# Kernel tuning notes

Measured on AMD Instinct MI355X. Metric: run time of the kernel, lower is better.

Reference implementation:

```python
import jax, jax.numpy as jnp
import numpy as np

B, S, HID = 2, 2048, 768
NH, HD = 12, 64
WINDOW_HALF = 64  # local_attention // 2
ROPE_THETA = 10000.0  # local_rope_theta (layer_id=1 -> local layer)


def setup_inputs() -> dict:
    key = jax.random.key(0)
    k1, k2, k3 = jax.random.split(key, 3)
    hidden_states = jax.random.normal(k1, (B, S, HID), dtype=jnp.float32)
    Wqkv_w = jax.random.normal(k2, (3 * HID, HID), dtype=jnp.float32) * (1.0 / np.sqrt(HID))
    Wo_w = jax.random.normal(k3, (HID, HID), dtype=jnp.float32) * (1.0 / np.sqrt(HID))
    # additive sliding-window mask: 0 inside +/-WINDOW_HALF band, finfo.min outside
    idx = jnp.arange(S)
    band = jnp.abs(idx[:, None] - idx[None, :]) <= WINDOW_HALF
    neg = jnp.finfo(jnp.float32).min
    sliding_window_mask = jnp.where(band, 0.0, neg)[None, None, :, :].astype(jnp.float32)
    position_ids = jnp.tile(jnp.arange(S, dtype=jnp.int64)[None, :], (B, 1))
    return {
        "hidden_states": hidden_states,
        "Wqkv_w": Wqkv_w,
        "Wo_w": Wo_w,
        "sliding_window_mask": sliding_window_mask,
        "position_ids": position_ids,
    }


def _rotate_half(x):
    x1, x2 = jnp.split(x, 2, axis=-1)
    return jnp.concatenate((-x2, x1), axis=-1)


def _rope_cos_sin(position_ids):
    # inv_freq: [HD//2]
    inv_freq = 1.0 / (ROPE_THETA ** (jnp.arange(0, HD, 2, dtype=jnp.float32) / HD))
    freqs = position_ids.astype(jnp.float32)[:, :, None] * inv_freq[None, None, :]  # [B,S,HD//2]
    emb = jnp.concatenate((freqs, freqs), axis=-1)  # [B,S,HD]
    return jnp.cos(emb), jnp.sin(emb)


def reference(hidden_states, Wqkv_w, Wo_w, sliding_window_mask, position_ids):
    bs, s, _ = hidden_states.shape
    qkv = hidden_states @ Wqkv_w.T  # [B,S,3*HID]
    qkv = qkv.reshape(bs, s, 3, NH, HD)
    # transpose(3,1).unbind(2) -> q,k,v each [B,NH,S,HD]
    qkv = jnp.transpose(qkv, (0, 3, 2, 1, 4))
    q, k, v = qkv[:, :, 0], qkv[:, :, 1], qkv[:, :, 2]
    cos, sin = _rope_cos_sin(position_ids)  # [B,S,HD]
    cos = cos[:, None, :, :].astype(hidden_states.dtype)
    sin = sin[:, None, :, :].astype(hidden_states.dtype)
    q = q * cos + _rotate_half(q) * sin
    k = k * cos + _rotate_half(k) * sin
    scale = 1.0 / np.sqrt(HD)
    scores = jnp.einsum("bhqd,bhkd->bhqk", q, k) * scale + sliding_window_mask
    probs = jax.nn.softmax(scores, axis=-1)
    attn = jnp.einsum("bhqk,bhkd->bhqd", probs, v)  # [B,NH,S,HD]
    attn = jnp.transpose(attn, (0, 2, 1, 3)).reshape(bs, s, NH * HD)
    return attn @ Wo_w.T
```

## Files before the change

### kernel.cpp

```cpp
#include <hip/hip_runtime.h>
#include <hip/hip_bf16.h>
#include <cstdint>

typedef __bf16 bf16_t;
typedef __bf16 bf16x8 __attribute__((ext_vector_type(8)));
typedef float f32x4 __attribute__((ext_vector_type(4)));

#define B_    2
#define S_    2048
#define HID_  768
#define NH_   12
#define HD_   64
#define KDIM_ 768

#define N_HID_  3145728
#define N_WQKV_ 1769472
#define N_WO_   589824

__device__ __forceinline__ void glds16(const bf16_t* g, const bf16_t* lds) {
  __builtin_amdgcn_global_load_lds((const __attribute__((address_space(1))) void*)g,
                                   (__attribute__((address_space(3))) void*)lds,
                                   16, 0, 0);
}

__global__ __launch_bounds__(256) void cvt3_kernel(
    const float* __restrict__ a, const float* __restrict__ b, const float* __restrict__ c,
    bf16_t* __restrict__ da, bf16_t* __restrict__ db, bf16_t* __restrict__ dc)
{
  size_t i = ((size_t)blockIdx.x * 256 + threadIdx.x) * 8;
  const float* s; bf16_t* d; size_t off;
  if (i < N_HID_)                { s = a; d = da; off = i; }
  else if (i < N_HID_ + N_WQKV_) { s = b; d = db; off = i - N_HID_; }
  else                           { s = c; d = dc; off = i - (N_HID_ + N_WQKV_); }
  float4 v0 = *(const float4*)(s + off);
  float4 v1 = *(const float4*)(s + off + 4);
  bf16x8 o;
  o[0] = (bf16_t)v0.x; o[1] = (bf16_t)v0.y; o[2] = (bf16_t)v0.z; o[3] = (bf16_t)v0.w;
  o[4] = (bf16_t)v1.x; o[5] = (bf16_t)v1.y; o[6] = (bf16_t)v1.z; o[7] = (bf16_t)v1.w;
  *(bf16x8*)(d + off) = o;
}

template<int MODE, int BM, int BN, int WM, int WN, int NTHR, int MINW, int NTX, int CHUNK>
__launch_bounds__(NTHR, MINW)
__global__ void gemm_kernel(const bf16_t* __restrict__ A,
                            const bf16_t* __restrict__ Bw,
                            bf16_t* __restrict__ Qo,
                            bf16_t* __restrict__ Ko,
                            bf16_t* __restrict__ Vo,
                            float* __restrict__ outf)
{
  constexpr int W    = WM * WN;
  constexpr int MACC = BM / WM / 16;
  constexpr int NWF  = BN / WN / 16;
  __shared__ bf16_t As[BM * 64];
  __shared__ bf16_t Bs[BN * 64];

  const int tid  = threadIdx.x;
  const int w    = tid >> 6;
  const int lane = tid & 63;
  const int wm   = w / WN, wn = w % WN;
  const int wk = (blockIdx.x & 7) * CHUNK + (blockIdx.x >> 3);
  const int tx = wk % NTX, ty = wk / NTX;
  const int m0 = ty * BM;
  const int n0 = tx * BN;
  const int lr  = lane >> 3;
  const int sub = lane & 7;

  f32x4 acc[MACC][NWF];
#pragma unroll
  for (int i = 0; i < MACC; i++)
#pragma unroll
    for (int j = 0; j < NWF; j++) acc[i][j] = f32x4{0.f, 0.f, 0.f, 0.f};

  for (int k0 = 0; k0 < KDIM_; k0 += 64) {
#pragma unroll
    for (int q = 0; q < BM / 8 / W; ++q) {
      const int rb = (q * W + w) * 8, row = rb + lr;
      glds16(A + (size_t)(m0 + row) * KDIM_ + k0 + (sub ^ (row & 7)) * 8, &As[rb * 64]);
    }
#pragma unroll
    for (int q = 0; q < BN / 8 / W; ++q) {
      const int rb = (q * W + w) * 8, row = rb + lr;
      glds16(Bw + (size_t)(n0 + row) * KDIM_ + k0 + (sub ^ (row & 7)) * 8, &Bs[rb * 64]);
    }
    __syncthreads();

#pragma unroll
    for (int kk = 0; kk < 2; ++kk) {
      const int su = kk * 4 + (lane >> 4);
      bf16x8 af[MACC], bfr[NWF];
#pragma unroll
      for (int m = 0; m < MACC; m++) {
        const int row = wm * (BM / WM) + m * 16 + (lane & 15);
        af[m] = *(const bf16x8*)&As[row * 64 + (su ^ (row & 7)) * 8];
      }
#pragma unroll
      for (int n = 0; n < NWF; n++) {
        const int row = wn * (BN / WN) + n * 16 + (lane & 15);
        bfr[n] = *(const bf16x8*)&Bs[row * 64 + (su ^ (row & 7)) * 8];
      }
      __builtin_amdgcn_s_setprio(1);
#pragma unroll
      for (int m = 0; m < MACC; m++)
#pragma unroll
        for (int n = 0; n < NWF; n++)
          acc[m][n] = __builtin_amdgcn_mfma_f32_16x16x32_bf16(af[m], bfr[n], acc[m][n], 0, 0, 0);
      __builtin_amdgcn_s_setprio(0);
    }
    if (k0 < KDIM_ - 64) __syncthreads();
  }

  const int c = lane & 15;
  if constexpr (MODE == 1) {
#pragma unroll
    for (int m = 0; m < MACC; m++)
#pragma unroll
      for (int r = 0; r < 4; r++) {
        const int row = m0 + wm * (BM / WM) + m * 16 + (lane >> 4) * 4 + r;
#pragma unroll
        for (int nf = 0; nf < NWF; nf++)
          outf[(size_t)row * HID_ + n0 + wn * (BN / WN) + nf * 16 + c] = acc[m][nf][r];
      }
  } else {
    const int slot  = tx * (BN / 64) + wn;
    const int which = slot / NH_;
    const int h     = slot % NH_;
    bf16_t* dst = (which == 0) ? Qo : (which == 1 ? Ko : Vo);
    const float NL = -13.287712379549449f / 32.0f;
    const float invf0 = exp2f((float)c * NL);
    const float invf1 = exp2f((float)(16 + c) * NL);
#pragma unroll
    for (int m = 0; m < MACC; m++)
#pragma unroll
      for (int r = 0; r < 4; r++) {
        const int row = m0 + wm * (BM / WM) + m * 16 + (lane >> 4) * 4 + r;
        const int b = row >> 11, s = row & 2047;
        const size_t base = ((size_t)(b * NH_ + h) * S_ + s) * HD_;
        if (which == 2) {
#pragma unroll
          for (int nf = 0; nf < 4; nf++)
            dst[base + nf * 16 + c] = (bf16_t)acc[m][nf][r];
        } else {
#pragma unroll
          for (int nf = 0; nf < 2; nf++) {
            float sn, cs;
            __sincosf((float)s * (nf ? invf1 : invf0), &sn, &cs);
            const float x1 = acc[m][nf][r], x2 = acc[m][nf + 2][r];
            dst[base + nf * 16 + c]      = (bf16_t)(x1 * cs - x2 * sn);
            dst[base + 32 + nf * 16 + c] = (bf16_t)(x2 * cs + x1 * sn);
          }
        }
      }
  }
}

__launch_bounds__(128, 4)
__global__ void attn_kernel(const bf16_t* __restrict__ Qw,
                            const bf16_t* __restrict__ Kw,
                            const bf16_t* __restrict__ Vw,
                            bf16_t* __restrict__ Ob)
{
  __shared__ bf16_t Vt[64 * 192];
  __shared__ bf16_t Pl[2][16 * 192];

  const int tid  = threadIdx.x;
  const int w    = tid >> 6;
  const int lane = tid & 63;
  const int bxq  = blockIdx.x;
  const int h    = blockIdx.y, b = blockIdx.z;
  const size_t base = (size_t)(b * NH_ + h) * S_ * HD_;
  const int kb = bxq * 32 - 64;

  const int i0 = bxq * 32 + w * 16;
  bf16x8 qf[2];
#pragma unroll
  for (int kk = 0; kk < 2; kk++)
    qf[kk] = *(const bf16x8*)(Qw + base + (size_t)(i0 + (lane & 15)) * HD_ + kk * 32 + (lane >> 4) * 8);

  {
#pragma unroll
    for (int it = 0; it < 10; ++it) {
      const int bk = it * 16 + (tid >> 3);
      const int d0 = (tid & 7) * 8;
      int j = kb + bk; j = j < 0 ? 0 : (j > S_ - 1 ? S_ - 1 : j);
      bf16x8 v = *(const bf16x8*)(Vw + base + (size_t)j * HD_ + d0);
      const int gsw = (((bk >> 3) ^ (tid & 7)) << 3) + (bk & 7);
#pragma unroll
      for (int e = 0; e < 8; e++) Vt[(d0 + e) * 192 + gsw] = v[e];
    }
    const bf16x8 z8 = {};
#pragma unroll
    for (int zz = 0; zz < 2; ++zz) {
      const int idx = zz * 128 + tid;
      const int d = idx >> 2, g = 20 + (idx & 3);
      *(bf16x8*)&Vt[d * 192 + ((g ^ (d >> 3)) << 3)] = z8;
    }
  }

  f32x4 sc[9];
#pragma unroll
  for (int t = 0; t < 9; t++) sc[t] = f32x4{0.f, 0.f, 0.f, 0.f};
#pragma unroll
  for (int kk = 0; kk < 2; kk++) {
    const int su = kk * 4 + (lane >> 4);
#pragma unroll
    for (int t = 0; t < 9; t++) {
      const int bk = w * 16 + t * 16 + (lane & 15);
      int j = kb + bk; j = j < 0 ? 0 : (j > S_ - 1 ? S_ - 1 : j);
      bf16x8 kf = *(const bf16x8*)(Kw + base + (size_t)j * HD_ + su * 8);
      sc[t] = __builtin_amdgcn_mfma_f32_16x16x32_bf16(qf[kk], kf, sc[t], 0, 0, 0);
    }
  }

  const int c  = lane & 15;
  const int qh = lane >> 4;
  float lrow[4];
#pragma unroll
  for (int r = 0; r < 4; r++) {
    const int i = i0 + qh * 4 + r;
    float mx = -1e30f;
#pragma unroll
    for (int t = 0; t < 9; t++) {
      const int j = kb + w * 16 + t * 16 + c;
      const int dd = j - i;
      const bool valid = (dd >= -64) && (dd <= 64) && (j >= 0) && (j < S_);
      const float v = valid ? sc[t][r] * 0.125f : -1e30f;
      sc[t][r] = v;
      mx = fmaxf(mx, v);
    }
    mx = fmaxf(mx, __shfl_xor(mx, 1, 16));
    mx = fmaxf(mx, __shfl_xor(mx, 2, 16));
    mx = fmaxf(mx, __shfl_xor(mx, 4, 16));
    mx = fmaxf(mx, __shfl_xor(mx, 8, 16));
    float sum = 0.f;
#pragma unroll
    for (int t = 0; t < 9; t++) {
      const float p = __expf(sc[t][r] - mx);
      sc[t][r] = p;
      sum += p;
    }
    sum += __shfl_xor(sum, 1, 16);
    sum += __shfl_xor(sum, 2, 16);
    sum += __shfl_xor(sum, 4, 16);
    sum += __shfl_xor(sum, 8, 16);
    lrow[r] = sum;
  }

#pragma unroll
  for (int t = 0; t < 9; t++)
#pragma unroll
    for (int r = 0; r < 4; r++) {
      const int row = qh * 4 + r;
      const int col = t * 16 + c;
      Pl[w][row * 192 + (((col >> 3) ^ (row & 7)) << 3) + (col & 7)] = (bf16_t)sc[t][r];
    }
  {
    const bf16x8 z8 = {};
    const int row = lane & 15, g = 18 + ((lane >> 4) & 1);
    *(bf16x8*)&Pl[w][row * 192 + ((g ^ (row & 7)) << 3)] = z8;
  }

  __syncthreads();

  f32x4 ao[4];
#pragma unroll
  for (int nf = 0; nf < 4; nf++) ao[nf] = f32x4{0.f, 0.f, 0.f, 0.f};
#pragma unroll
  for (int kc = 0; kc < 5; kc++) {
    const int prow = lane & 15;
    const int Lp = kc * 32 + (lane >> 4) * 8;
    bf16x8 pf = *(const bf16x8*)&Pl[w][prow * 192 + (((Lp >> 3) ^ (prow & 7)) << 3)];
#pragma unroll
    for (int nf = 0; nf < 4; nf++) {
      const int d = nf * 16 + (lane & 15);
      const int L = w * 16 + Lp;
      bf16x8 vf = *(const bf16x8*)&Vt[d * 192 + (((L >> 3) ^ (d >> 3)) << 3)];
      ao[nf] = __builtin_amdgcn_mfma_f32_16x16x32_bf16(pf, vf, ao[nf], 0, 0, 0);
    }
  }

#pragma unroll
  for (int r = 0; r < 4; r++) {
    const float inv = 1.0f / lrow[r];
    const int srow = i0 + qh * 4 + r;
    const size_t orow = ((size_t)(b * S_ + srow)) * HID_ + h * HD_;
#pragma unroll
    for (int nf = 0; nf < 4; nf++)
      Ob[orow + nf * 16 + c] = (bf16_t)(ao[nf][r] * inv);
  }
}

extern "C" void kernel_launch(void* const* d_in, const int* in_sizes, int n_in,
                              void* d_out, int out_size, void* d_ws, size_t ws_size,
                              hipStream_t stream) {
  const float* hidden_f = (const float*)d_in[0];
  const float* wqkv_f   = (const float*)d_in[1];
  const float* wo_f     = (const float*)d_in[2];

  bf16_t* ws = (bf16_t*)d_ws;
  size_t off = 0;
  bf16_t* Hb    = ws + off; off += N_HID_;
  bf16_t* Wqkvb = ws + off; off += N_WQKV_;
  bf16_t* Wob   = ws + off; off += N_WO_;
  const size_t E = (size_t)B_ * NH_ * S_ * HD_;
  bf16_t* Q    = ws + off; off += E;
  bf16_t* K    = ws + off; off += E;
  bf16_t* V    = ws + off; off += E;
  bf16_t* ABUF = ws + off; off += E;
  float*  out  = (float*)d_out;

  cvt3_kernel<<<dim3((N_HID_ + N_WQKV_ + N_WO_) / (256 * 8)), dim3(256), 0, stream>>>(
      hidden_f, wqkv_f, wo_f, Hb, Wqkvb, Wob);
  gemm_kernel<0, 128, 128, 4, 2, 512, 4, 18, 72><<<dim3(576), dim3(512), 0, stream>>>(
      Hb, Wqkvb, Q, K, V, nullptr);
  attn_kernel<<<dim3(64, 12, 2), dim3(128), 0, stream>>>(Q, K, V, ABUF);
  gemm_kernel<1, 64, 64, 2, 2, 256, 4, 12, 96><<<dim3(768), dim3(256), 0, stream>>>(
      ABUF, Wob, nullptr, nullptr, nullptr, out);
}
```

Before: 62.50 us.

## Prefetch next K-tile into registers while computing current tile in GEMM

Replaces direct global-to-LDS async loads with register-staged loads: the next K tile is fetched into registers before the MFMA compute on the current tile, then written to LDS after a barrier. The aim is to overlap global memory latency with MFMA work within a single LDS buffer. In exchange it uses more VGPRs and adds an extra barrier per iteration, and it gives up the global_load_lds path that bypasses registers. The K loop is also fully unrolled.

```diff
diff --git a/kernel.cpp b/kernel.cpp
--- a/kernel.cpp
+++ b/kernel.cpp
@@ -16,12 +16,6 @@
 #define N_HID_  3145728
 #define N_WQKV_ 1769472
 #define N_WO_   589824
-
-__device__ __forceinline__ void glds16(const bf16_t* g, const bf16_t* lds) {
-  __builtin_amdgcn_global_load_lds((const __attribute__((address_space(1))) void*)g,
-                                   (__attribute__((address_space(3))) void*)lds,
-                                   16, 0, 0);
-}
 
 __global__ __launch_bounds__(256) void cvt3_kernel(
     const float* __restrict__ a, const float* __restrict__ b, const float* __restrict__ c,
@@ -52,6 +46,9 @@
   constexpr int W    = WM * WN;
   constexpr int MACC = BM / WM / 16;
   constexpr int NWF  = BN / WN / 16;
+  constexpr int AW   = BM / 8 / W;
+  constexpr int BW   = BN / 8 / W;
+  constexpr int NT   = KDIM_ / 64;
   __shared__ bf16_t As[BM * 64];
   __shared__ bf16_t Bs[BN * 64];
 
@@ -72,19 +69,34 @@
 #pragma unroll
     for (int j = 0; j < NWF; j++) acc[i][j] = f32x4{0.f, 0.f, 0.f, 0.f};
 
-  for (int k0 = 0; k0 < KDIM_; k0 += 64) {
-#pragma unroll
-    for (int q = 0; q < BM / 8 / W; ++q) {
-      const int rb = (q * W + w) * 8, row = rb + lr;
-      glds16(A + (size_t)(m0 + row) * KDIM_ + k0 + (sub ^ (row & 7)) * 8, &As[rb * 64]);
-    }
-#pragma unroll
-    for (int q = 0; q < BN / 8 / W; ++q) {
-      const int rb = (q * W + w) * 8, row = rb + lr;
-      glds16(Bw + (size_t)(n0 + row) * KDIM_ + k0 + (sub ^ (row & 7)) * 8, &Bs[rb * 64]);
-    }
-    __syncthreads();
-
+  bf16x8 rA[AW], rB[BW];
+
+  auto STAGE_LOAD = [&](int k0) {
+#pragma unroll
+    for (int q = 0; q < AW; ++q) {
+      const int row = (q * W + w) * 8 + lr;
+      rA[q] = *(const bf16x8*)(A + (size_t)(m0 + row) * KDIM_ + k0 + (sub ^ (row & 7)) * 8);
+    }
+#pragma unroll
+    for (int q = 0; q < BW; ++q) {
+      const int row = (q * W + w) * 8 + lr;
+      rB[q] = *(const bf16x8*)(Bw + (size_t)(n0 + row) * KDIM_ + k0 + (sub ^ (row & 7)) * 8);
+    }
+  };
+  auto STAGE_WRITE = [&]() {
+#pragma unroll
+    for (int q = 0; q < AW; ++q) {
+      const int rb = (q * W + w) * 8;
+      *(bf16x8*)&As[rb * 64 + lane * 8] = rA[q];
+    }
+#pragma unroll
+    for (int q = 0; q < BW; ++q) {
+      const int rb = (q * W + w) * 8;
+      *(bf16x8*)&Bs[rb * 64 + lane * 8] = rB[q];
+    }
+  };
+
+  auto COMPUTE = [&]() {
 #pragma unroll
     for (int kk = 0; kk < 2; ++kk) {
       const int su = kk * 4 + (lane >> 4);
@@ -107,7 +119,20 @@
           acc[m][n] = __builtin_amdgcn_mfma_f32_16x16x32_bf16(af[m], bfr[n], acc[m][n], 0, 0, 0);
       __builtin_amdgcn_s_setprio(0);
     }
-    if (k0 < KDIM_ - 64) __syncthreads();
+  };
+
+  STAGE_LOAD(0);
+  STAGE_WRITE();
+  __syncthreads();
+#pragma unroll
+  for (int t = 0; t < NT; ++t) {
+    if (t < NT - 1) STAGE_LOAD((t + 1) * 64);
+    COMPUTE();
+    if (t < NT - 1) {
+      __syncthreads();
+      STAGE_WRITE();
+      __syncthreads();
+    }
   }
 
   const int c = lane & 15;
```

Result: slower. 65.24 us (+4.4%).
